# Kernel optimization log

Measured on AMD Instinct MI355X. Metric: run time of the kernel, lower is better.

## Reference

```python
import jax, jax.numpy as jnp
import numpy as np

ALPHA = 0.2
SIGMA_IN = 0.2
B, T, N, IN = 128, 512, 512, 6

def setup_inputs() -> dict:
    key = jax.random.key(0)
    k1, k2, k3, k4, k5, k6 = jax.random.split(key, 6)
    u = jax.random.normal(k1, (B, T, IN), dtype=jnp.float32)
    input_noise = jax.random.normal(k2, (B, T, IN), dtype=jnp.float32)
    recurrent_noise = jax.random.normal(k3, (B, T, N), dtype=jnp.float32)
    # recurrent_layer: Linear(n, n) with diagonal filled to 0.2
    W_rec = jax.random.normal(k4, (N, N), dtype=jnp.float32) / np.sqrt(N)
    W_rec = W_rec.at[jnp.arange(N), jnp.arange(N)].set(0.2)
    # bias initialized normal(mean=0.2, std=0) -> constant 0.2, frozen
    b_rec = jnp.full((N,), 0.2, dtype=jnp.float32)
    W_in = jax.random.normal(k5, (N, IN), dtype=jnp.float32) / np.sqrt(IN)
    return {"u": u, "input_noise": input_noise, "recurrent_noise": recurrent_noise,
            "W_rec": W_rec, "b_rec": b_rec, "W_in": W_in}

def reference(u, input_noise, recurrent_noise, W_rec, b_rec, W_in):
    alpha = jnp.float32(ALPHA)
    noise_scale = jnp.sqrt(jnp.float32(2.0 / ALPHA) * jnp.float32(SIGMA_IN) ** 2)
    # inputs = input_layer(u + scaled_noise): [B,T,N]
    inputs = jnp.einsum('bti,ni->btn', u + noise_scale * input_noise, W_in)
    b, t, _ = u.shape
    n = W_rec.shape[0]
    # scan over the first t-1 steps (state 0 is zeros, states has length t)
    inp_t = jnp.swapaxes(inputs[:, :t - 1], 0, 1)            # [T-1, B, N]
    rn_t = jnp.swapaxes(recurrent_noise[:, :t - 1], 0, 1)    # [T-1, B, N]
    h0 = jnp.zeros((b, n), dtype=u.dtype)

    def step(h, xs):
        inp, rn = xs
        pre = h @ W_rec.T + b_rec + inp
        h_new = (1.0 - alpha) * h + alpha * (jax.nn.relu(pre) + rn)
        return h_new, h_new

    _, hs = jax.lax.scan(step, h0, (inp_t, rn_t))            # [T-1, B, N]
    states = jnp.concatenate([h0[None], hs], axis=0)          # [T, B, N]
    return jnp.swapaxes(states, 0, 1)                         # [B, T, N]
```

## Files before the change

kernel.cpp:

```cpp
#include <hip/hip_runtime.h>


#define B_  128
#define T_  512
#define N_  512
#define IN_ 6

typedef _Float16 f16x8 __attribute__((ext_vector_type(8)));
typedef float    f32x4 __attribute__((ext_vector_type(4)));
typedef _Float16 h2_t  __attribute__((ext_vector_type(2)));

union U4H8 { uint4 u; f16x8 h; };
__device__ __forceinline__ f16x8 h8(uint4 v) { U4H8 c; c.u = v; return c.h; }

__device__ __forceinline__ uint4 pack8(const float* __restrict__ p) {
    const float4 f0 = ((const float4*)p)[0];
    const float4 f1 = ((const float4*)p)[1];
    union { unsigned u[4]; h2_t h[4]; } cv;
    cv.h[0] = h2_t{(_Float16)f0.x, (_Float16)f0.y};
    cv.h[1] = h2_t{(_Float16)f0.z, (_Float16)f0.w};
    cv.h[2] = h2_t{(_Float16)f1.x, (_Float16)f1.y};
    cv.h[3] = h2_t{(_Float16)f1.z, (_Float16)f1.w};
    return uint4{cv.u[0], cv.u[1], cv.u[2], cv.u[3]};
}

#define KEEP4(v) asm volatile("" : "+v"((v).x), "+v"((v).y), "+v"((v).z), "+v"((v).w))

#define MFMA(A, Bv, C) __builtin_amdgcn_mfma_f32_16x16x32_f16(h8(A), h8(Bv), (C), 0, 0, 0)

__global__ void prep_tail_kernel(const float* __restrict__ Wrec,
                                 uint4* __restrict__ ws) {
    int tid = blockIdx.x * blockDim.x + threadIdx.x;
    if (tid >= 36 * N_) return;
    int g = tid >> 9, n = tid & (N_ - 1);
    ws[(size_t)g * N_ + n] = pack8(Wrec + (size_t)n * N_ + 224 + 8 * g);
}

template <bool USE_WS>
__device__ __forceinline__ uint4 sld(const uint4* __restrict__ wsb,
                                     const float* __restrict__ Wrec,
                                     int rowA, int q, int KK, int T) {
    if constexpr (USE_WS) return wsb[2048 * (KK - 7) + 16 * T];
    else return pack8(Wrec + (size_t)(rowA + 16 * T) * N_ + 32 * KK + 8 * q);
}

template <bool USE_WS>
__global__ __launch_bounds__(512)
void rnn_scan_kernel(
    const float* __restrict__ u,
    const float* __restrict__ unz,
    const float* __restrict__ rnz,
    const float* __restrict__ Wrec,
    const float* __restrict__ brec,
    const float* __restrict__ Win,
    const uint4* __restrict__ ws,
    float* __restrict__ out)
{
    const int b    = blockIdx.x;
    const int n    = threadIdx.x;
    const int w    = n >> 6;
    const int lane = n & 63;
    const int q    = lane >> 4;
    const int r16  = lane & 15;

    __shared__ uint4 lw[16 * N_];
    __shared__ __align__(16) _Float16 hbuf[2][N_];
    __shared__ float pre[N_];

    const int rowA = 64 * w + r16;
    const float* wp = Wrec + (size_t)rowA * N_ + 8 * q;

    uint4 a00 = pack8(wp +     0 +  0), a01 = pack8(wp +     0 + 32), a02 = pack8(wp +     0 + 64);
    uint4 a10 = pack8(wp +  8192 +  0), a11 = pack8(wp +  8192 + 32), a12 = pack8(wp +  8192 + 64);
    uint4 a20 = pack8(wp + 16384 +  0), a21 = pack8(wp + 16384 + 32), a22 = pack8(wp + 16384 + 64);
    uint4 a30 = pack8(wp + 24576 +  0), a31 = pack8(wp + 24576 + 32), a32 = pack8(wp + 24576 + 64);
    KEEP4(a00); KEEP4(a01); KEEP4(a02); KEEP4(a10); KEEP4(a11); KEEP4(a12);
    KEEP4(a20); KEEP4(a21); KEEP4(a22); KEEP4(a30); KEEP4(a31); KEEP4(a32);

#pragma unroll
    for (int j = 0; j < 16; ++j)
        lw[j * N_ + n] = pack8(Wrec + (size_t)n * N_ + 96 + 8 * j);

    const float win0 = Win[n * IN_ + 0], win1 = Win[n * IN_ + 1], win2 = Win[n * IN_ + 2];
    const float win3 = Win[n * IN_ + 3], win4 = Win[n * IN_ + 4], win5 = Win[n * IN_ + 5];
    const float br = brec[n];
    const float NS = 0.6324555320336759f;
    float h = 0.0f;

    float* ob = out + (size_t)b * T_ * N_;
    const float* rb = rnz + (size_t)b * T_ * N_;
    const float2* ubp = (const float2*)(u   + (size_t)b * T_ * IN_);
    const float2* nbp = (const float2*)(unz + (size_t)b * T_ * IN_);

    const uint4* wsb = nullptr;
    if constexpr (USE_WS) wsb = ws + (size_t)q * N_ + 64 * w + r16;
    const int lbase = q * N_ + 64 * w + r16;
    const uint4* hb0 = (const uint4*)&hbuf[0][0];
    const uint4* hb1 = (const uint4*)&hbuf[1][0];

    hbuf[0][n] = (_Float16)0.0f;

    float2 cu0 = ubp[0], cu1 = ubp[1], cu2 = ubp[2];
    float2 cn0 = nbp[0], cn1 = nbp[1], cn2 = nbp[2];
    float inp_c = br;
    inp_c = fmaf(win0, fmaf(NS, cn0.x, cu0.x), inp_c);
    inp_c = fmaf(win1, fmaf(NS, cn0.y, cu0.y), inp_c);
    inp_c = fmaf(win2, fmaf(NS, cn1.x, cu1.x), inp_c);
    inp_c = fmaf(win3, fmaf(NS, cn1.y, cu1.y), inp_c);
    inp_c = fmaf(win4, fmaf(NS, cn2.x, cu2.x), inp_c);
    inp_c = fmaf(win5, fmaf(NS, cn2.y, cu2.y), inp_c);
    float rn_c = rb[n];
    __syncthreads();

#pragma unroll 1
    for (int t = 0; t < T_ - 1; ++t) {
        ob[(size_t)t * N_ + n] = h;

        const uint4* hb = (t & 1) ? hb1 : hb0;
        _Float16* hbw = (t & 1) ? &hbuf[0][0] : &hbuf[1][0];

        uint4 bf0 = hb[q], bf1 = hb[4 + q];

        uint4 sa0 = sld<USE_WS>(wsb, Wrec, rowA, q, 7, 0), sa1 = sld<USE_WS>(wsb, Wrec, rowA, q, 7, 1),
              sa2 = sld<USE_WS>(wsb, Wrec, rowA, q, 7, 2), sa3 = sld<USE_WS>(wsb, Wrec, rowA, q, 7, 3);
        uint4 sb0 = sld<USE_WS>(wsb, Wrec, rowA, q, 8, 0), sb1 = sld<USE_WS>(wsb, Wrec, rowA, q, 8, 1),
              sb2 = sld<USE_WS>(wsb, Wrec, rowA, q, 8, 2), sb3 = sld<USE_WS>(wsb, Wrec, rowA, q, 8, 3);

        const float rn_n = rb[(size_t)(t + 1) * N_ + n];
        const float2 pu0 = ubp[(t + 1) * 3 + 0], pu1 = ubp[(t + 1) * 3 + 1], pu2 = ubp[(t + 1) * 3 + 2];
        const float2 pn0 = nbp[(t + 1) * 3 + 0], pn1 = nbp[(t + 1) * 3 + 1], pn2 = nbp[(t + 1) * 3 + 2];

        const f32x4 zz = {0.0f, 0.0f, 0.0f, 0.0f};

        uint4 bf2 = hb[8 + q];
        f32x4 d0 = MFMA(a00, bf0, zz), d1 = MFMA(a10, bf0, zz),
              d2 = MFMA(a20, bf0, zz), d3 = MFMA(a30, bf0, zz);
        uint4 bf3 = hb[12 + q];
        d0 = MFMA(a01, bf1, d0); d1 = MFMA(a11, bf1, d1);
        d2 = MFMA(a21, bf1, d2); d3 = MFMA(a31, bf1, d3);
        uint4 bf4 = hb[16 + q];
        d0 = MFMA(a02, bf2, d0); d1 = MFMA(a12, bf2, d1);
        d2 = MFMA(a22, bf2, d2); d3 = MFMA(a32, bf2, d3);

        uint4 l30 = lw[lbase + 0], l31 = lw[lbase + 16], l32 = lw[lbase + 32], l33 = lw[lbase + 48];
        uint4 bf5 = hb[20 + q];
        d0 = MFMA(l30, bf3, d0); d1 = MFMA(l31, bf3, d1);
        d2 = MFMA(l32, bf3, d2); d3 = MFMA(l33, bf3, d3);
        uint4 l40 = lw[lbase + 2048], l41 = lw[lbase + 2064], l42 = lw[lbase + 2080], l43 = lw[lbase + 2096];
        uint4 bf6 = hb[24 + q];
        d0 = MFMA(l40, bf4, d0); d1 = MFMA(l41, bf4, d1);
        d2 = MFMA(l42, bf4, d2); d3 = MFMA(l43, bf4, d3);
        uint4 l50 = lw[lbase + 4096], l51 = lw[lbase + 4112], l52 = lw[lbase + 4128], l53 = lw[lbase + 4144];
        uint4 bf7 = hb[28 + q];
        d0 = MFMA(l50, bf5, d0); d1 = MFMA(l51, bf5, d1);
        d2 = MFMA(l52, bf5, d2); d3 = MFMA(l53, bf5, d3);
        uint4 l60 = lw[lbase + 6144], l61 = lw[lbase + 6160], l62 = lw[lbase + 6176], l63 = lw[lbase + 6192];
        uint4 bf8 = hb[32 + q];
        d0 = MFMA(l60, bf6, d0); d1 = MFMA(l61, bf6, d1);
        d2 = MFMA(l62, bf6, d2); d3 = MFMA(l63, bf6, d3);

        uint4 bf9 = hb[36 + q];
        d0 = MFMA(sa0, bf7, d0); d1 = MFMA(sa1, bf7, d1);
        d2 = MFMA(sa2, bf7, d2); d3 = MFMA(sa3, bf7, d3);
        sa0 = sld<USE_WS>(wsb, Wrec, rowA, q, 9, 0); sa1 = sld<USE_WS>(wsb, Wrec, rowA, q, 9, 1);
        sa2 = sld<USE_WS>(wsb, Wrec, rowA, q, 9, 2); sa3 = sld<USE_WS>(wsb, Wrec, rowA, q, 9, 3);

        uint4 bf10 = hb[40 + q];
        d0 = MFMA(sb0, bf8, d0); d1 = MFMA(sb1, bf8, d1);
        d2 = MFMA(sb2, bf8, d2); d3 = MFMA(sb3, bf8, d3);
        sb0 = sld<USE_WS>(wsb, Wrec, rowA, q, 10, 0); sb1 = sld<USE_WS>(wsb, Wrec, rowA, q, 10, 1);
        sb2 = sld<USE_WS>(wsb, Wrec, rowA, q, 10, 2); sb3 = sld<USE_WS>(wsb, Wrec, rowA, q, 10, 3);

        uint4 bf11 = hb[44 + q];
        d0 = MFMA(sa0, bf9, d0); d1 = MFMA(sa1, bf9, d1);
        d2 = MFMA(sa2, bf9, d2); d3 = MFMA(sa3, bf9, d3);
        sa0 = sld<USE_WS>(wsb, Wrec, rowA, q, 11, 0); sa1 = sld<USE_WS>(wsb, Wrec, rowA, q, 11, 1);
        sa2 = sld<USE_WS>(wsb, Wrec, rowA, q, 11, 2); sa3 = sld<USE_WS>(wsb, Wrec, rowA, q, 11, 3);

        uint4 bf12 = hb[48 + q];
        d0 = MFMA(sb0, bf10, d0); d1 = MFMA(sb1, bf10, d1);
        d2 = MFMA(sb2, bf10, d2); d3 = MFMA(sb3, bf10, d3);
        sb0 = sld<USE_WS>(wsb, Wrec, rowA, q, 12, 0); sb1 = sld<USE_WS>(wsb, Wrec, rowA, q, 12, 1);
        sb2 = sld<USE_WS>(wsb, Wrec, rowA, q, 12, 2); sb3 = sld<USE_WS>(wsb, Wrec, rowA, q, 12, 3);

        uint4 bf13 = hb[52 + q];
        d0 = MFMA(sa0, bf11, d0); d1 = MFMA(sa1, bf11, d1);
        d2 = MFMA(sa2, bf11, d2); d3 = MFMA(sa3, bf11, d3);
        sa0 = sld<USE_WS>(wsb, Wrec, rowA, q, 13, 0); sa1 = sld<USE_WS>(wsb, Wrec, rowA, q, 13, 1);
        sa2 = sld<USE_WS>(wsb, Wrec, rowA, q, 13, 2); sa3 = sld<USE_WS>(wsb, Wrec, rowA, q, 13, 3);

        uint4 bf14 = hb[56 + q];
        d0 = MFMA(sb0, bf12, d0); d1 = MFMA(sb1, bf12, d1);
        d2 = MFMA(sb2, bf12, d2); d3 = MFMA(sb3, bf12, d3);
        sb0 = sld<USE_WS>(wsb, Wrec, rowA, q, 14, 0); sb1 = sld<USE_WS>(wsb, Wrec, rowA, q, 14, 1);
        sb2 = sld<USE_WS>(wsb, Wrec, rowA, q, 14, 2); sb3 = sld<USE_WS>(wsb, Wrec, rowA, q, 14, 3);

        uint4 bf15 = hb[60 + q];
        d0 = MFMA(sa0, bf13, d0); d1 = MFMA(sa1, bf13, d1);
        d2 = MFMA(sa2, bf13, d2); d3 = MFMA(sa3, bf13, d3);
        sa0 = sld<USE_WS>(wsb, Wrec, rowA, q, 15, 0); sa1 = sld<USE_WS>(wsb, Wrec, rowA, q, 15, 1);
        sa2 = sld<USE_WS>(wsb, Wrec, rowA, q, 15, 2); sa3 = sld<USE_WS>(wsb, Wrec, rowA, q, 15, 3);

        d0 = MFMA(sb0, bf14, d0); d1 = MFMA(sb1, bf14, d1);
        d2 = MFMA(sb2, bf14, d2); d3 = MFMA(sb3, bf14, d3);

        d0 = MFMA(sa0, bf15, d0); d1 = MFMA(sa1, bf15, d1);
        d2 = MFMA(sa2, bf15, d2); d3 = MFMA(sa3, bf15, d3);

        if (r16 == 0) {
            *(f32x4*)(pre + 64 * w +  0 + 4 * q) = d0;
            *(f32x4*)(pre + 64 * w + 16 + 4 * q) = d1;
            *(f32x4*)(pre + 64 * w + 32 + 4 * q) = d2;
            *(f32x4*)(pre + 64 * w + 48 + 4 * q) = d3;
        }
        __syncthreads();

        const float prn = pre[n] + inp_c;
        h = 0.8f * h + 0.2f * (fmaxf(prn, 0.0f) + rn_c);
        hbw[n] = (_Float16)h;

        float inp_n = br;
        inp_n = fmaf(win0, fmaf(NS, pn0.x, pu0.x), inp_n);
        inp_n = fmaf(win1, fmaf(NS, pn0.y, pu0.y), inp_n);
        inp_n = fmaf(win2, fmaf(NS, pn1.x, pu1.x), inp_n);
        inp_n = fmaf(win3, fmaf(NS, pn1.y, pu1.y), inp_n);
        inp_n = fmaf(win4, fmaf(NS, pn2.x, pu2.x), inp_n);
        inp_n = fmaf(win5, fmaf(NS, pn2.y, pu2.y), inp_n);
        inp_c = inp_n;
        rn_c  = rn_n;
        __syncthreads();
    }
    ob[(size_t)(T_ - 1) * N_ + n] = h;
}

extern "C" void kernel_launch(void* const* d_in, const int* in_sizes, int n_in,
                              void* d_out, int out_size, void* d_ws, size_t ws_size,
                              hipStream_t stream) {
    const float* u    = (const float*)d_in[0];
    const float* unz  = (const float*)d_in[1];
    const float* rnz  = (const float*)d_in[2];
    const float* Wrec = (const float*)d_in[3];
    const float* brec = (const float*)d_in[4];
    const float* Win  = (const float*)d_in[5];
    float* out = (float*)d_out;

    const size_t ws_need = (size_t)36 * N_ * sizeof(uint4);
    if (ws_size >= ws_need) {
        uint4* ws = (uint4*)d_ws;
        prep_tail_kernel<<<(36 * N_ + 255) / 256, 256, 0, stream>>>(Wrec, ws);
        rnn_scan_kernel<true><<<dim3(B_), dim3(512), 0, stream>>>(
            u, unz, rnz, Wrec, brec, Win, ws, out);
    } else {
        rnn_scan_kernel<false><<<dim3(B_), dim3(512), 0, stream>>>(
            u, unz, rnz, Wrec, brec, Win, nullptr, out);
    }
}
```

Baseline: 940.6 us.

## Apply state update in MFMA owner lanes and drop second barrier

The kernel no longer stages the matmul result through a shared 'pre' buffer and runs the elementwise update across all threads. Lanes that hold accumulator rows (r16<4) now compute input projection, ReLU, leaky update, output store and fp16 state write directly from the MFMA registers, with W_in and bias staged in LDS. This removes one __syncthreads and an LDS round trip per timestep. In exchange only a quarter of lanes do the elementwise work, each handling four outputs, and the input projection is recomputed per step inside the MFMA chain.

```diff
diff --git a/kernel.cpp b/kernel.cpp
--- a/kernel.cpp
+++ b/kernel.cpp
@@ -65,7 +65,8 @@
 
     __shared__ uint4 lw[16 * N_];
     __shared__ __align__(16) _Float16 hbuf[2][N_];
-    __shared__ float pre[N_];
+    __shared__ __align__(16) float winl[N_ * 8];
+    __shared__ __align__(16) float brl[N_];
 
     const int rowA = 64 * w + r16;
     const float* wp = Wrec + (size_t)rowA * N_ + 8 * q;
@@ -81,11 +82,13 @@
     for (int j = 0; j < 16; ++j)
         lw[j * N_ + n] = pack8(Wrec + (size_t)n * N_ + 96 + 8 * j);
 
-    const float win0 = Win[n * IN_ + 0], win1 = Win[n * IN_ + 1], win2 = Win[n * IN_ + 2];
-    const float win3 = Win[n * IN_ + 3], win4 = Win[n * IN_ + 4], win5 = Win[n * IN_ + 5];
-    const float br = brec[n];
+    winl[n * 8 + 0] = Win[n * IN_ + 0]; winl[n * 8 + 1] = Win[n * IN_ + 1];
+    winl[n * 8 + 2] = Win[n * IN_ + 2]; winl[n * 8 + 3] = Win[n * IN_ + 3];
+    winl[n * 8 + 4] = Win[n * IN_ + 4]; winl[n * 8 + 5] = Win[n * IN_ + 5];
+    winl[n * 8 + 6] = 0.0f;             winl[n * 8 + 7] = 0.0f;
+    brl[n] = brec[n];
+
     const float NS = 0.6324555320336759f;
-    float h = 0.0f;
 
     float* ob = out + (size_t)b * T_ * N_;
     const float* rb = rnz + (size_t)b * T_ * N_;
@@ -98,26 +101,18 @@
     const uint4* hb0 = (const uint4*)&hbuf[0][0];
     const uint4* hb1 = (const uint4*)&hbuf[1][0];
 
+    const bool owner = (r16 < 4);
+    const int rowO = 64 * w + 16 * r16 + 4 * q;
+    float h0 = 0.0f, h1 = 0.0f, h2 = 0.0f, h3 = 0.0f;
+
     hbuf[0][n] = (_Float16)0.0f;
-
-    float2 cu0 = ubp[0], cu1 = ubp[1], cu2 = ubp[2];
-    float2 cn0 = nbp[0], cn1 = nbp[1], cn2 = nbp[2];
-    float inp_c = br;
-    inp_c = fmaf(win0, fmaf(NS, cn0.x, cu0.x), inp_c);
-    inp_c = fmaf(win1, fmaf(NS, cn0.y, cu0.y), inp_c);
-    inp_c = fmaf(win2, fmaf(NS, cn1.x, cu1.x), inp_c);
-    inp_c = fmaf(win3, fmaf(NS, cn1.y, cu1.y), inp_c);
-    inp_c = fmaf(win4, fmaf(NS, cn2.x, cu2.x), inp_c);
-    inp_c = fmaf(win5, fmaf(NS, cn2.y, cu2.y), inp_c);
-    float rn_c = rb[n];
+    hbuf[1][n] = (_Float16)0.0f;
+    ob[n] = 0.0f;
     __syncthreads();
 
 #pragma unroll 1
     for (int t = 0; t < T_ - 1; ++t) {
-        ob[(size_t)t * N_ + n] = h;
-
         const uint4* hb = (t & 1) ? hb1 : hb0;
-        _Float16* hbw = (t & 1) ? &hbuf[0][0] : &hbuf[1][0];
 
         uint4 bf0 = hb[q], bf1 = hb[4 + q];
 
@@ -126,9 +121,13 @@
         uint4 sb0 = sld<USE_WS>(wsb, Wrec, rowA, q, 8, 0), sb1 = sld<USE_WS>(wsb, Wrec, rowA, q, 8, 1),
               sb2 = sld<USE_WS>(wsb, Wrec, rowA, q, 8, 2), sb3 = sld<USE_WS>(wsb, Wrec, rowA, q, 8, 3);
 
-        const float rn_n = rb[(size_t)(t + 1) * N_ + n];
-        const float2 pu0 = ubp[(t + 1) * 3 + 0], pu1 = ubp[(t + 1) * 3 + 1], pu2 = ubp[(t + 1) * 3 + 2];
-        const float2 pn0 = nbp[(t + 1) * 3 + 0], pn1 = nbp[(t + 1) * 3 + 1], pn2 = nbp[(t + 1) * 3 + 2];
+        float4 rn4{0,0,0,0};
+        float2 uu0{0,0}, uu1{0,0}, uu2{0,0}, nu0{0,0}, nu1{0,0}, nu2{0,0};
+        if (owner) {
+            rn4 = *(const float4*)(rb + (size_t)t * N_ + rowO);
+            uu0 = ubp[t * 3 + 0]; uu1 = ubp[t * 3 + 1]; uu2 = ubp[t * 3 + 2];
+            nu0 = nbp[t * 3 + 0]; nu1 = nbp[t * 3 + 1]; nu2 = nbp[t * 3 + 2];
+        }
 
         const f32x4 zz = {0.0f, 0.0f, 0.0f, 0.0f};
 
@@ -141,6 +140,23 @@
         uint4 bf4 = hb[16 + q];
         d0 = MFMA(a02, bf2, d0); d1 = MFMA(a12, bf2, d1);
         d2 = MFMA(a22, bf2, d2); d3 = MFMA(a32, bf2, d3);
+
+        float i0 = 0.0f, i1 = 0.0f, i2 = 0.0f, i3 = 0.0f;
+        if (owner) {
+            const float c0 = fmaf(NS, nu0.x, uu0.x), c1 = fmaf(NS, nu0.y, uu0.y);
+            const float c2 = fmaf(NS, nu1.x, uu1.x), c3 = fmaf(NS, nu1.y, uu1.y);
+            const float c4 = fmaf(NS, nu2.x, uu2.x), c5 = fmaf(NS, nu2.y, uu2.y);
+            const float4 b4 = *(const float4*)&brl[rowO];
+#pragma unroll
+            for (int r = 0; r < 4; ++r) {
+                const float4 wA = *(const float4*)&winl[(rowO + r) * 8];
+                const float2 wB = *(const float2*)&winl[(rowO + r) * 8 + 4];
+                float v = (r == 0) ? b4.x : (r == 1) ? b4.y : (r == 2) ? b4.z : b4.w;
+                v = fmaf(wA.x, c0, v); v = fmaf(wA.y, c1, v); v = fmaf(wA.z, c2, v);
+                v = fmaf(wA.w, c3, v); v = fmaf(wB.x, c4, v); v = fmaf(wB.y, c5, v);
+                if (r == 0) i0 = v; else if (r == 1) i1 = v; else if (r == 2) i2 = v; else i3 = v;
+            }
+        }
 
         uint4 l30 = lw[lbase + 0], l31 = lw[lbase + 16], l32 = lw[lbase + 32], l33 = lw[lbase + 48];
         uint4 bf5 = hb[20 + q];
@@ -207,30 +223,20 @@
         d0 = MFMA(sa0, bf15, d0); d1 = MFMA(sa1, bf15, d1);
         d2 = MFMA(sa2, bf15, d2); d3 = MFMA(sa3, bf15, d3);
 
-        if (r16 == 0) {
-            *(f32x4*)(pre + 64 * w +  0 + 4 * q) = d0;
-            *(f32x4*)(pre + 64 * w + 16 + 4 * q) = d1;
-            *(f32x4*)(pre + 64 * w + 32 + 4 * q) = d2;
-            *(f32x4*)(pre + 64 * w + 48 + 4 * q) = d3;
+        if (owner) {
+            const f32x4 dd = (r16 == 0) ? d0 : (r16 == 1) ? d1 : (r16 == 2) ? d2 : d3;
+            h0 = 0.8f * h0 + 0.2f * (fmaxf(dd[0] + i0, 0.0f) + rn4.x);
+            h1 = 0.8f * h1 + 0.2f * (fmaxf(dd[1] + i1, 0.0f) + rn4.y);
+            h2 = 0.8f * h2 + 0.2f * (fmaxf(dd[2] + i2, 0.0f) + rn4.z);
+            h3 = 0.8f * h3 + 0.2f * (fmaxf(dd[3] + i3, 0.0f) + rn4.w);
+            *(float4*)(ob + (size_t)(t + 1) * N_ + rowO) = float4{h0, h1, h2, h3};
+            union { uint2 u2; h2_t h[2]; } pk;
+            pk.h[0] = h2_t{(_Float16)h0, (_Float16)h1};
+            pk.h[1] = h2_t{(_Float16)h2, (_Float16)h3};
+            *(uint2*)(&hbuf[(t + 1) & 1][rowO]) = pk.u2;
         }
         __syncthreads();
-
-        const float prn = pre[n] + inp_c;
-        h = 0.8f * h + 0.2f * (fmaxf(prn, 0.0f) + rn_c);
-        hbw[n] = (_Float16)h;
-
-        float inp_n = br;
-        inp_n = fmaf(win0, fmaf(NS, pn0.x, pu0.x), inp_n);
-        inp_n = fmaf(win1, fmaf(NS, pn0.y, pu0.y), inp_n);
-        inp_n = fmaf(win2, fmaf(NS, pn1.x, pu1.x), inp_n);
-        inp_n = fmaf(win3, fmaf(NS, pn1.y, pu1.y), inp_n);
-        inp_n = fmaf(win4, fmaf(NS, pn2.x, pu2.x), inp_n);
-        inp_n = fmaf(win5, fmaf(NS, pn2.y, pu2.y), inp_n);
-        inp_c = inp_n;
-        rn_c  = rn_n;
-        __syncthreads();
     }
-    ob[(size_t)(T_ - 1) * N_ + n] = h;
 }
 
 extern "C" void kernel_launch(void* const* d_in, const int* in_sizes, int n_in,
```

Measured after the change: 1.520 ms. +61.6%, slower.
